# Performance work log

Measured on AMD Instinct MI355X. Metric: run time of the kernel, lower is better.

The kernel has to match this reference:

```python
import jax, jax.numpy as jnp
import numpy as np

B, N, E = 8, 20000, 320000
T, A, P = 4000, 8000, 8000
F_IN, C = 128, 128
N1 = N + 1  # row 0 is a reserved zero/eps node


def setup_inputs() -> dict:
    key = jax.random.key(0)
    ks = jax.random.split(key, 20)
    xn = lambda k, s: jax.random.normal(k, s, dtype=jnp.float32)

    def lin(k, i, o):
        k1, k2 = jax.random.split(k)
        s = (2.0 / (i + o)) ** 0.5  # xavier_normal as in the torch init
        return xn(k1, (i, o)) * s, xn(k2, (o,)) * 0.01

    inp = {}
    inp["topic_emb"] = xn(ks[0], (B, T, 130))
    inp["au_emb"] = xn(ks[1], (B, A, 37))
    inp["paper_emb"] = xn(ks[2], (B, P, 289))
    # disjoint node-id sets covering rows 1..N of feat
    inp["topic_set"] = jnp.broadcast_to(jnp.arange(1, T + 1), (B, T))
    inp["author_set"] = jnp.broadcast_to(jnp.arange(T + 1, T + A + 1), (B, A))
    inp["paper_set"] = jnp.broadcast_to(jnp.arange(T + A + 1, N + 1), (B, P))
    inp["edge_index"] = jax.random.randint(ks[3], (B, 2, E), 1, N + 1)
    inp["topic_id"] = jax.random.randint(ks[4], (B, 50), 1, T + 1)
    inp["author_id"] = jax.random.randint(ks[5], (B, 20), T + 1, T + A + 1)
    inp["topic_cnt"] = jnp.full((B,), 50.0, dtype=jnp.float32)
    inp["auth_cnt"] = jnp.full((B,), 20.0, dtype=jnp.float32)
    # learned params (stored as [in, out], i.e. torch W transposed)
    inp["W_topic"], inp["b_topic"] = lin(ks[6], 130, F_IN)
    inp["W_au"], inp["b_au"] = lin(ks[7], 37, F_IN)
    inp["W_paper"], inp["b_paper"] = lin(ks[8], 289, F_IN)
    inp["gat_W"] = xn(ks[9], (F_IN, C)) * (2.0 / (F_IN + C)) ** 0.5
    inp["att_src"] = xn(ks[10], (C,)) * 0.1
    inp["att_dst"] = xn(ks[11], (C,)) * 0.1
    inp["gat_b"] = jnp.zeros((C,), dtype=jnp.float32)
    inp["W1"], inp["b1"] = lin(ks[12], 3 * C, 2 * C)
    inp["W2"], inp["b2"] = lin(ks[13], 2 * C, C)
    inp["W3"], inp["b3"] = lin(ks[14], C, 1)
    return inp


def reference(topic_emb, au_emb, paper_emb, topic_cnt, auth_cnt,
              W_topic, b_topic, W_au, b_au, W_paper, b_paper,
              gat_W, att_src, att_dst, gat_b,
              W1, b1, W2, b2, W3, b3,
              topic_set, author_set, paper_set, edge_index, topic_id, author_id):
    # eval mode: all dropouts are identity
    t_f = topic_emb @ W_topic + b_topic    # [B,T,F]
    a_f = au_emb @ W_au + b_au             # [B,A,F]
    p_f = paper_emb @ W_paper + b_paper    # [B,P,F]
    loop_idx = jnp.arange(N1)

    def per_graph(tf, af, pf, tset, aset, pset, ei, tid, aid, tcnt, acnt):
        feat = jnp.zeros((N1, F_IN), dtype=tf.dtype)
        feat = feat.at[tset].set(tf).at[aset].set(af).at[pset].set(pf)
        # --- GATConv (heads=1, PyG semantics, self-loops added) ---
        x = feat @ gat_W  # [N1, C]
        src = jnp.concatenate([ei[0], loop_idx])
        dst = jnp.concatenate([ei[1], loop_idx])
        e = jax.nn.leaky_relu((x @ att_src)[src] + (x @ att_dst)[dst], 0.2)
        emax = jax.ops.segment_max(e, dst, num_segments=N1)  # softmax over dst neighborhoods
        ee = jnp.exp(e - emax[dst])
        denom = jax.ops.segment_sum(ee, dst, num_segments=N1) + 1e-16
        out = jax.ops.segment_sum(ee[:, None] * x[src], dst, num_segments=N1) / denom[:, None] + gat_b
        h = jax.nn.relu(out)
        h = h.at[0].set(1e-5)
        # --- gather-sum pooling ---
        t_pool = h[tid].sum(0) / (1e-5 + tcnt)               # [C]
        af2 = h[aid]                                          # [n_auth, C]
        a_pool = jnp.concatenate([af2[0], af2[1:].sum(0) / (-1.00001 + acnt)])  # [2C]
        return jnp.concatenate([a_pool, t_pool])              # [3C]

    cat = jax.vmap(per_graph)(t_f, a_f, p_f, topic_set, author_set, paper_set,
                              edge_index, topic_id, author_id, topic_cnt, auth_cnt)
    h = jnp.tanh(cat @ W1 + b1)
    h = jnp.tanh(h @ W2 + b2)
    return (h @ W3 + b3).reshape(-1)
```

## Files before the change

### kernel.cpp

```cpp
#include <hip/hip_runtime.h>
#include <math.h>

#define BB 8
#define N1 20001
#define TT 4000
#define AAU 8000
#define PP 8000
#define EE 320000
#define CC 128
#define KT 130
#define KA 37
#define KP 289
#define ROWS (KT + KA + KP)
#define CAP 96
#define NS 70
#define EB 128

__device__ __forceinline__ void node_ref(int node, int& t, int& K, int& base, int& row) {
    if (node <= TT)            { t = 0; K = KT; base = 0;        row = node - 1; }
    else if (node <= TT + AAU) { t = 1; K = KA; base = KT;       row = node - TT - 1; }
    else                       { t = 2; K = KP; base = KT + KA;  row = node - TT - AAU - 1; }
}

__device__ __forceinline__ int typ3(int id) { return id <= TT ? 0 : (id <= TT + AAU ? 1 : 2); }
__device__ __forceinline__ float lrelu02(float v) { return v >= 0.f ? v : 0.2f * v; }
__device__ __forceinline__ unsigned hashid(int id) { return (((unsigned)id * 2654435761u) >> 22) & 511u; }

template <int K>
__device__ __forceinline__ float dotK(const float* __restrict__ er,
                                      const float* __restrict__ u, int l) {
    float p = 0.f;
#pragma unroll
    for (int j = 0; j < (K + 63) / 64; ++j) {
        int k = l + 64 * j;
        if (k < K) p += er[k] * u[k];
    }
    return p;
}

template <int K>
__device__ __forceinline__ void dot2K(const float* __restrict__ er,
                                      const float* __restrict__ ul,
                                      const float* __restrict__ udg, int l,
                                      float& ps, float& pd) {
#pragma unroll
    for (int j = 0; j < (K + 63) / 64; ++j) {
        int k = l + 64 * j;
        if (k < K) { float v = er[k]; ps += v * ul[k]; pd += v * udg[k]; }
    }
}

template <int K>
__device__ __forceinline__ void accK(const float* __restrict__ er,
                                     float* __restrict__ z, float w, int l) {
#pragma unroll
    for (int j = 0; j < (K + 63) / 64; ++j) {
        int k = l + 64 * j;
        if (k < K) atomicAdd(&z[k], w * er[k]);
    }
}

__global__ void __launch_bounds__(512)
kPrep(const float* __restrict__ Wt, const float* __restrict__ Wa, const float* __restrict__ Wpp,
      const float* __restrict__ bt, const float* __restrict__ ba, const float* __restrict__ bpw,
      const float* __restrict__ gatW, const float* __restrict__ attS, const float* __restrict__ attD,
      const int* __restrict__ topic_id, const int* __restrict__ author_id,
      float* __restrict__ Wp, float* __restrict__ bp,
      float* __restrict__ u_src, float* __restrict__ u_dst, float* __restrict__ c_sd,
      int* __restrict__ slot_node, int* __restrict__ tid_slot, int* __restrict__ aid_slot,
      int* __restrict__ cnt2) {
    __shared__ int hkey[512], hval[512];
    __shared__ float redS[8], redD[8];
    int bid = blockIdx.x, tid = threadIdx.x;
    if (bid < 115) {
        int c = tid & 127;
        int r = bid * 4 + (tid >> 7);
        float acc = 0.f;
        const float* wrow = nullptr;
        if (r < KT)            wrow = Wt  + (size_t)r * CC;
        else if (r < KT + KA)  wrow = Wa  + (size_t)(r - KT) * CC;
        else if (r < ROWS)     wrow = Wpp + (size_t)(r - KT - KA) * CC;
        else if (r == ROWS)     wrow = bt;
        else if (r == ROWS + 1) wrow = ba;
        else if (r == ROWS + 2) wrow = bpw;
        if (wrow) {
#pragma unroll 16
            for (int j = 0; j < CC; ++j) acc += wrow[j] * gatW[j * CC + c];
            if (r < ROWS) Wp[r * CC + c] = acc;
            else          bp[(r - ROWS) * CC + c] = acc;
        }
        float ps = acc * attS[c], pd = acc * attD[c];
        for (int o = 32; o; o >>= 1) { ps += __shfl_down(ps, o); pd += __shfl_down(pd, o); }
        int w = tid >> 6;
        if ((tid & 63) == 0) { redS[w] = ps; redD[w] = pd; }
        __syncthreads();
        if (tid < 4) {
            int r2 = bid * 4 + tid;
            float us = redS[2 * tid] + redS[2 * tid + 1];
            float ud = redD[2 * tid] + redD[2 * tid + 1];
            if (r2 < ROWS)          { u_src[r2] = us; u_dst[r2] = ud; }
            else if (r2 < ROWS + 3) { c_sd[r2 - ROWS] = us; c_sd[3 + r2 - ROWS] = ud; }
        }
    } else {
        int b = bid - 115;
        for (int i = tid; i < 512; i += 512) { hkey[i] = -1; hval[i] = 0x7fffffff; }
        if (tid < NS) cnt2[b * NS + tid] = 0;
        __syncthreads();
        int id = -1, cell = -1;
        if (tid < NS) {
            id = (tid < 50) ? topic_id[b * 50 + tid] : author_id[b * 20 + tid - 50];
            unsigned h = hashid(id);
            while (true) {
                int old = atomicCAS(&hkey[h], -1, id);
                if (old == -1 || old == id) { cell = (int)h; break; }
                h = (h + 1) & 511u;
            }
            atomicMin(&hval[cell], tid);
        }
        __syncthreads();
        if (tid < NS) {
            int winner = hval[cell];
            if (tid < 50) tid_slot[b * 50 + tid] = winner;
            else          aid_slot[b * 20 + tid - 50] = winner;
            slot_node[b * NS + tid] = (winner == tid) ? id : -1;
        }
    }
}

__global__ void __launch_bounds__(256)
kEdges(const int* __restrict__ edge_index, const int* __restrict__ slot_node,
       int* __restrict__ cnt2, int* __restrict__ entry_src) {
    __shared__ int htab[512];
    int bid = blockIdx.x, b = bid >> 7, chunk = bid & 127, tid = threadIdx.x;
    for (int i = tid; i < 512; i += 256) htab[i] = -1;
    __syncthreads();
    if (tid < NS) {
        int id = slot_node[b * NS + tid];
        if (id >= 0) {
            unsigned h = hashid(id);
            while (atomicCAS(&htab[h], -1, (id << 7) | tid) != -1) h = (h + 1) & 511u;
        }
    }
    __syncthreads();
    const int* dsts  = edge_index + (size_t)b * 2 * EE + EE;
    const int* srcsg = edge_index + (size_t)b * 2 * EE;
    const int per = EE / EB;
    int e0 = chunk * per;
    for (int e = e0 + tid; e < e0 + per; e += 256) {
        int dst = dsts[e];
        unsigned h = hashid(dst);
        int slot = -1;
        while (true) {
            int v = htab[h];
            if (v == -1) break;
            if ((v >> 7) == dst) { slot = v & 127; break; }
            h = (h + 1) & 511u;
        }
        if (slot >= 0) {
            int pos = atomicAdd(&cnt2[b * NS + slot], 1);
            if (pos < CAP) entry_src[(size_t)(b * NS + slot) * CAP + pos] = srcsg[e];
        }
    }
}

__global__ void __launch_bounds__(512)
kAgg(const float* __restrict__ temb, const float* __restrict__ aemb,
     const float* __restrict__ pemb,
     const int* __restrict__ slot_node, const int* __restrict__ cnt2,
     const int* __restrict__ entry_src,
     const float* __restrict__ u_src, const float* __restrict__ u_dst,
     const float* __restrict__ c_sd,
     const float* __restrict__ Wp, const float* __restrict__ bp,
     const float* __restrict__ gatB, float* __restrict__ h_slot) {
    __shared__ float u_l[ROWS], e_l[CAP], w_l[CAP], z_l[ROWS], red_l[4 * CC];
    __shared__ float sw_l[3], s_denom, s_wself, s_asrc, s_adraw;
    int bid = blockIdx.x, b = bid / NS;
    int node = slot_node[bid];
    if (node < 0) return;
    int tid = threadIdx.x, wv = tid >> 6, l = tid & 63;
    int deg = cnt2[bid]; if (deg > CAP) deg = CAP;
    const int* srcs = entry_src + (size_t)bid * CAP;
    const float* tb = temb + (size_t)b * TT * KT;
    const float* ab = aemb + (size_t)b * AAU * KA;
    const float* pb = pemb + (size_t)b * PP * KP;

    for (int i = tid; i < ROWS; i += 512) { u_l[i] = u_src[i]; z_l[i] = 0.f; }
    __syncthreads();

    for (int i = wv; i <= deg; i += 8) {
        int src = (i < deg) ? srcs[i] : node;
        int t, K, base, row; node_ref(src, t, K, base, row);
        const float* er = (t == 0) ? tb + (size_t)row * KT
                        : (t == 1) ? ab + (size_t)row * KA
                                   : pb + (size_t)row * KP;
        if (i < deg) {
            float p;
            if (t == 0)      p = dotK<KT>(er, u_l, l);
            else if (t == 1) p = dotK<KA>(er, u_l + KT, l);
            else             p = dotK<KP>(er, u_l + KT + KA, l);
            for (int o = 32; o; o >>= 1) p += __shfl_down(p, o);
            if (l == 0) e_l[i] = p + c_sd[t];
        } else {
            float ps = 0.f, pd = 0.f;
            if (t == 0)      dot2K<KT>(er, u_l, u_dst, l, ps, pd);
            else if (t == 1) dot2K<KA>(er, u_l + KT, u_dst + KT, l, ps, pd);
            else             dot2K<KP>(er, u_l + KT + KA, u_dst + KT + KA, l, ps, pd);
            for (int o = 32; o; o >>= 1) { ps += __shfl_down(ps, o); pd += __shfl_down(pd, o); }
            if (l == 0) { s_asrc = ps + c_sd[t]; s_adraw = pd + c_sd[3 + t]; }
        }
    }
    __syncthreads();

    if (wv == 0) {
        float adst = s_adraw;
        float es = lrelu02(s_asrc + adst);
        float v0 = (l < deg) ? lrelu02(e_l[l] + adst) : -1e30f;
        float v1 = (l + 64 < deg) ? lrelu02(e_l[l + 64] + adst) : -1e30f;
        float m = fmaxf(v0, v1);
        for (int o = 32; o; o >>= 1) m = fmaxf(m, __shfl_down(m, o));
        m = fmaxf(__shfl(m, 0), es);
        float w0 = 0.f, w1 = 0.f;
        int t0 = 0, t1 = 0;
        if (l < deg)      { w0 = expf(v0 - m); w_l[l] = w0;      t0 = typ3(srcs[l]); }
        if (l + 64 < deg) { w1 = expf(v1 - m); w_l[l + 64] = w1; t1 = typ3(srcs[l + 64]); }
        float s0 = 0.f, s1 = 0.f, s2 = 0.f, d = w0 + w1;
        if (t0 == 0) s0 += w0; else if (t0 == 1) s1 += w0; else s2 += w0;
        if (t1 == 0) s0 += w1; else if (t1 == 1) s1 += w1; else s2 += w1;
        for (int o = 32; o; o >>= 1) {
            d  += __shfl_down(d, o);
            s0 += __shfl_down(s0, o);
            s1 += __shfl_down(s1, o);
            s2 += __shfl_down(s2, o);
        }
        if (l == 0) {
            float ws = expf(es - m);
            d += ws;
            int tn = typ3(node);
            if (tn == 0) s0 += ws; else if (tn == 1) s1 += ws; else s2 += ws;
            sw_l[0] = s0; sw_l[1] = s1; sw_l[2] = s2;
            s_denom = d + 1e-16f;
            s_wself = ws;
        }
    }
    __syncthreads();

    for (int i = wv; i <= deg; i += 8) {
        int src; float w;
        if (i < deg) { src = srcs[i]; w = w_l[i]; }
        else         { src = node;    w = s_wself; }
        int t, K, base, row; node_ref(src, t, K, base, row);
        if (t == 0)      accK<KT>(tb + (size_t)row * KT, z_l, w, l);
        else if (t == 1) accK<KA>(ab + (size_t)row * KA, z_l + KT, w, l);
        else             accK<KP>(pb + (size_t)row * KP, z_l + KT + KA, w, l);
    }
    __syncthreads();

    {
        int kc = tid >> 7, c = tid & 127;
        const int kb = kc * 114, ke = kb + 114;
        float p = 0.f;
#pragma unroll 8
        for (int k = kb; k < ke; ++k) p += z_l[k] * Wp[k * CC + c];
        red_l[kc * CC + c] = p;
    }
    __syncthreads();
    if (tid < CC) {
        float num = red_l[tid] + red_l[CC + tid] + red_l[2 * CC + tid] + red_l[3 * CC + tid];
        num += sw_l[0] * bp[tid] + sw_l[1] * bp[CC + tid] + sw_l[2] * bp[2 * CC + tid];
        float h = num / s_denom + gatB[tid];
        h_slot[(size_t)bid * CC + tid] = h > 0.f ? h : 0.f;
    }
}

__global__ void __launch_bounds__(512)
kPool(const float* __restrict__ h_slot, const int* __restrict__ tid_slot,
      const int* __restrict__ aid_slot,
      const float* __restrict__ tcnt, const float* __restrict__ acnt,
      const float* __restrict__ W1, const float* __restrict__ b1,
      const float* __restrict__ W2, const float* __restrict__ b2,
      const float* __restrict__ W3, const float* __restrict__ b3,
      float* __restrict__ out) {
    __shared__ float cat_l[384], h1_l[256], h2_l[128], redA[2 * 256], redB[4 * 128];
    int b = blockIdx.x, tid = threadIdx.x;
    if (tid < 128) {
        cat_l[tid] = h_slot[(size_t)(b * NS + aid_slot[b * 20]) * CC + tid];
    } else if (tid < 256) {
        int t = tid - 128;
        float ap = 0.f;
        for (int j = 1; j < 20; ++j) ap += h_slot[(size_t)(b * NS + aid_slot[b * 20 + j]) * CC + t];
        cat_l[128 + t] = ap / (acnt[b] - 1.00001f);
    } else if (tid < 384) {
        int t = tid - 256;
        float tp = 0.f;
        for (int j = 0; j < 50; ++j) tp += h_slot[(size_t)(b * NS + tid_slot[b * 50 + j]) * CC + t];
        cat_l[256 + t] = tp / (1e-5f + tcnt[b]);
    }
    __syncthreads();
    {
        int c = tid & 255, half = tid >> 8;
        const int kb = half * 192, ke = kb + 192;
        float acc = 0.f;
#pragma unroll 8
        for (int k = kb; k < ke; ++k) acc += cat_l[k] * W1[k * 256 + c];
        redA[half * 256 + c] = acc;
    }
    __syncthreads();
    if (tid < 256) h1_l[tid] = tanhf(b1[tid] + redA[tid] + redA[256 + tid]);
    __syncthreads();
    {
        int c = tid & 127, q = tid >> 7;
        const int kb = q * 64, ke = kb + 64;
        float acc = 0.f;
#pragma unroll 8
        for (int k = kb; k < ke; ++k) acc += h1_l[k] * W2[k * CC + c];
        redB[q * CC + c] = acc;
    }
    __syncthreads();
    if (tid < 128) {
        float v = tanhf(b2[tid] + redB[tid] + redB[CC + tid] + redB[2 * CC + tid] + redB[3 * CC + tid]);
        h2_l[tid] = v * W3[tid];
    }
    __syncthreads();
    if (tid < 64) {
        float s = h2_l[tid] + h2_l[tid + 64];
        for (int o = 32; o; o >>= 1) s += __shfl_down(s, o);
        if (tid == 0) out[b] = s + b3[0];
    }
}

extern "C" void kernel_launch(void* const* d_in, const int* in_sizes, int n_in,
                              void* d_out, int out_size, void* d_ws, size_t ws_size,
                              hipStream_t stream) {
    const float* temb = (const float*)d_in[0];
    const float* aemb = (const float*)d_in[1];
    const float* pemb = (const float*)d_in[2];
    const int* edge_index = (const int*)d_in[6];
    const int* topic_id   = (const int*)d_in[7];
    const int* author_id  = (const int*)d_in[8];
    const float* tcnt = (const float*)d_in[9];
    const float* acnt = (const float*)d_in[10];
    const float* Wt  = (const float*)d_in[11];
    const float* bt  = (const float*)d_in[12];
    const float* Wa  = (const float*)d_in[13];
    const float* ba  = (const float*)d_in[14];
    const float* Wpw = (const float*)d_in[15];
    const float* bpw = (const float*)d_in[16];
    const float* gatW = (const float*)d_in[17];
    const float* attS = (const float*)d_in[18];
    const float* attD = (const float*)d_in[19];
    const float* gatB = (const float*)d_in[20];
    const float* W1 = (const float*)d_in[21];
    const float* b1 = (const float*)d_in[22];
    const float* W2 = (const float*)d_in[23];
    const float* b2 = (const float*)d_in[24];
    const float* W3 = (const float*)d_in[25];
    const float* b3 = (const float*)d_in[26];

    char* ws = (char*)d_ws;
    size_t off = 0;
    auto alloc = [&](size_t bytes) -> void* {
        void* p = ws + off;
        off = (off + bytes + 255) & ~(size_t)255;
        return p;
    };
    float* Wp      = (float*)alloc((size_t)ROWS * CC * 4);
    float* bp      = (float*)alloc(3 * CC * 4);
    float* u_src   = (float*)alloc(ROWS * 4);
    float* u_dst   = (float*)alloc(ROWS * 4);
    float* c_sd    = (float*)alloc(6 * 4);
    int* slot_node = (int*)alloc(BB * NS * 4);
    int* tid_slot  = (int*)alloc(BB * 50 * 4);
    int* aid_slot  = (int*)alloc(BB * 20 * 4);
    int* cnt2      = (int*)alloc(BB * NS * 4);
    int* entry_src = (int*)alloc((size_t)BB * NS * CAP * 4);
    float* h_slot  = (float*)alloc((size_t)BB * NS * CC * 4);
    (void)ws_size; (void)in_sizes; (void)n_in; (void)out_size;

    kPrep<<<dim3(115 + BB), dim3(512), 0, stream>>>(Wt, Wa, Wpw, bt, ba, bpw, gatW, attS, attD,
                                                    topic_id, author_id,
                                                    Wp, bp, u_src, u_dst, c_sd,
                                                    slot_node, tid_slot, aid_slot, cnt2);
    kEdges<<<dim3(BB * EB), dim3(256), 0, stream>>>(edge_index, slot_node, cnt2, entry_src);
    kAgg<<<dim3(BB * NS), dim3(512), 0, stream>>>(temb, aemb, pemb, slot_node, cnt2, entry_src,
                                                  u_src, u_dst, c_sd, Wp, bp, gatB, h_slot);
    kPool<<<dim3(BB), dim3(512), 0, stream>>>(h_slot, tid_slot, aid_slot, tcnt, acnt,
                                              W1, b1, W2, b2, W3, b3, (float*)d_out);
}
```

Measured before the change: 65.29 us.

## Fuse GAT pipeline into two kernels with per-chunk edge bins and single-pass softmax

Four launches become two. Edge binning moves into the prep kernel: each edge block rebuilds the slot hash table locally and counts into shared-memory bins per chunk, which removes the global atomics on cnt2. Aggregation computes exp weights in a single pass without subtracting the segment max, keeps each row in registers for both the dot product and the weighted accumulation, and fuses the pooling MLP through a last-block-done counter. This cuts launch gaps and extra passes over rows, at the risk of exp overflow for large attention logits and of dropping edges if a chunk bin exceeds 12 entries.

```diff
diff --git a/kernel.cpp b/kernel.cpp
--- a/kernel.cpp
+++ b/kernel.cpp
@@ -2,7 +2,6 @@
 #include <math.h>
 
 #define BB 8
-#define N1 20001
 #define TT 4000
 #define AAU 8000
 #define PP 8000
@@ -11,10 +10,12 @@
 #define KT 130
 #define KA 37
 #define KP 289
-#define ROWS (KT + KA + KP)
-#define CAP 96
+#define ROWS 456
 #define NS 70
-#define EB 128
+#define EBK 64
+#define EPC (EE/EBK)
+#define CAPC 12
+#define NWB 115
 
 __device__ __forceinline__ void node_ref(int node, int& t, int& K, int& base, int& row) {
     if (node <= TT)            { t = 0; K = KT; base = 0;        row = node - 1; }
@@ -22,64 +23,60 @@
     else                       { t = 2; K = KP; base = KT + KA;  row = node - TT - AAU - 1; }
 }
 
-__device__ __forceinline__ int typ3(int id) { return id <= TT ? 0 : (id <= TT + AAU ? 1 : 2); }
 __device__ __forceinline__ float lrelu02(float v) { return v >= 0.f ? v : 0.2f * v; }
 __device__ __forceinline__ unsigned hashid(int id) { return (((unsigned)id * 2654435761u) >> 22) & 511u; }
 
 template <int K>
-__device__ __forceinline__ float dotK(const float* __restrict__ er,
-                                      const float* __restrict__ u, int l) {
+__device__ __forceinline__ void loadRow(const float* __restrict__ er, int l, float* v) {
+#pragma unroll
+    for (int j = 0; j < (K + 63) / 64; ++j) {
+        int k = l + 64 * j;
+        v[j] = (k < K) ? er[k] : 0.f;
+    }
+}
+
+template <int K>
+__device__ __forceinline__ float dotRegs(const float* v, const float* __restrict__ u, int l) {
     float p = 0.f;
 #pragma unroll
     for (int j = 0; j < (K + 63) / 64; ++j) {
         int k = l + 64 * j;
-        if (k < K) p += er[k] * u[k];
+        if (k < K) p += v[j] * u[k];
     }
     return p;
 }
 
 template <int K>
-__device__ __forceinline__ void dot2K(const float* __restrict__ er,
-                                      const float* __restrict__ ul,
-                                      const float* __restrict__ udg, int l,
-                                      float& ps, float& pd) {
+__device__ __forceinline__ void accRegs(const float* v, float* __restrict__ z, float w, int l) {
 #pragma unroll
     for (int j = 0; j < (K + 63) / 64; ++j) {
         int k = l + 64 * j;
-        if (k < K) { float v = er[k]; ps += v * ul[k]; pd += v * udg[k]; }
-    }
-}
-
-template <int K>
-__device__ __forceinline__ void accK(const float* __restrict__ er,
-                                     float* __restrict__ z, float w, int l) {
-#pragma unroll
-    for (int j = 0; j < (K + 63) / 64; ++j) {
-        int k = l + 64 * j;
-        if (k < K) atomicAdd(&z[k], w * er[k]);
+        if (k < K) atomicAdd(&z[k], w * v[j]);
     }
 }
 
 __global__ void __launch_bounds__(512)
-kPrep(const float* __restrict__ Wt, const float* __restrict__ Wa, const float* __restrict__ Wpp,
-      const float* __restrict__ bt, const float* __restrict__ ba, const float* __restrict__ bpw,
-      const float* __restrict__ gatW, const float* __restrict__ attS, const float* __restrict__ attD,
-      const int* __restrict__ topic_id, const int* __restrict__ author_id,
-      float* __restrict__ Wp, float* __restrict__ bp,
-      float* __restrict__ u_src, float* __restrict__ u_dst, float* __restrict__ c_sd,
-      int* __restrict__ slot_node, int* __restrict__ tid_slot, int* __restrict__ aid_slot,
-      int* __restrict__ cnt2) {
-    __shared__ int hkey[512], hval[512];
+k1(const float* __restrict__ Wt, const float* __restrict__ Wa, const float* __restrict__ Wpp,
+   const float* __restrict__ bt, const float* __restrict__ ba, const float* __restrict__ bpw,
+   const float* __restrict__ gatW, const float* __restrict__ attS, const float* __restrict__ attD,
+   const int* __restrict__ topic_id, const int* __restrict__ author_id,
+   const int* __restrict__ edge_index,
+   float* __restrict__ Wp, float* __restrict__ bp,
+   float* __restrict__ u_src, float* __restrict__ u_dst, float* __restrict__ c_sd,
+   int* __restrict__ slot_node, int* __restrict__ tid_slot, int* __restrict__ aid_slot,
+   int* __restrict__ cnt2, int* __restrict__ entry_src, int* __restrict__ done) {
+    __shared__ int hkey[512], hval[512], lcnt[NS];
     __shared__ float redS[8], redD[8];
     int bid = blockIdx.x, tid = threadIdx.x;
-    if (bid < 115) {
+
+    if (bid < NWB) {
         int c = tid & 127;
         int r = bid * 4 + (tid >> 7);
         float acc = 0.f;
         const float* wrow = nullptr;
-        if (r < KT)            wrow = Wt  + (size_t)r * CC;
-        else if (r < KT + KA)  wrow = Wa  + (size_t)(r - KT) * CC;
-        else if (r < ROWS)     wrow = Wpp + (size_t)(r - KT - KA) * CC;
+        if (r < KT)             wrow = Wt  + (size_t)r * CC;
+        else if (r < KT + KA)   wrow = Wa  + (size_t)(r - KT) * CC;
+        else if (r < ROWS)      wrow = Wpp + (size_t)(r - KT - KA) * CC;
         else if (r == ROWS)     wrow = bt;
         else if (r == ROWS + 1) wrow = ba;
         else if (r == ROWS + 2) wrow = bpw;
@@ -101,10 +98,10 @@
             if (r2 < ROWS)          { u_src[r2] = us; u_dst[r2] = ud; }
             else if (r2 < ROWS + 3) { c_sd[r2 - ROWS] = us; c_sd[3 + r2 - ROWS] = ud; }
         }
-    } else {
-        int b = bid - 115;
+    } else if (bid < NWB + BB) {
+        int b = bid - NWB;
         for (int i = tid; i < 512; i += 512) { hkey[i] = -1; hval[i] = 0x7fffffff; }
-        if (tid < NS) cnt2[b * NS + tid] = 0;
+        if (tid == 0) done[b] = 0;
         __syncthreads();
         int id = -1, cell = -1;
         if (tid < NS) {
@@ -124,207 +121,194 @@
             else          aid_slot[b * 20 + tid - 50] = winner;
             slot_node[b * NS + tid] = (winner == tid) ? id : -1;
         }
-    }
-}
-
-__global__ void __launch_bounds__(256)
-kEdges(const int* __restrict__ edge_index, const int* __restrict__ slot_node,
-       int* __restrict__ cnt2, int* __restrict__ entry_src) {
-    __shared__ int htab[512];
-    int bid = blockIdx.x, b = bid >> 7, chunk = bid & 127, tid = threadIdx.x;
-    for (int i = tid; i < 512; i += 256) htab[i] = -1;
-    __syncthreads();
-    if (tid < NS) {
-        int id = slot_node[b * NS + tid];
-        if (id >= 0) {
+    } else {
+        int eb = bid - NWB - BB;
+        int b = eb / EBK, chunk = eb % EBK;
+        for (int i = tid; i < 512; i += 512) { hkey[i] = -1; hval[i] = 0x7fffffff; }
+        if (tid < NS) lcnt[tid] = 0;
+        __syncthreads();
+        if (tid < NS) {
+            int id = (tid < 50) ? topic_id[b * 50 + tid] : author_id[b * 20 + tid - 50];
             unsigned h = hashid(id);
-            while (atomicCAS(&htab[h], -1, (id << 7) | tid) != -1) h = (h + 1) & 511u;
-        }
-    }
-    __syncthreads();
-    const int* dsts  = edge_index + (size_t)b * 2 * EE + EE;
-    const int* srcsg = edge_index + (size_t)b * 2 * EE;
-    const int per = EE / EB;
-    int e0 = chunk * per;
-    for (int e = e0 + tid; e < e0 + per; e += 256) {
-        int dst = dsts[e];
-        unsigned h = hashid(dst);
-        int slot = -1;
-        while (true) {
-            int v = htab[h];
-            if (v == -1) break;
-            if ((v >> 7) == dst) { slot = v & 127; break; }
-            h = (h + 1) & 511u;
-        }
-        if (slot >= 0) {
-            int pos = atomicAdd(&cnt2[b * NS + slot], 1);
-            if (pos < CAP) entry_src[(size_t)(b * NS + slot) * CAP + pos] = srcsg[e];
+            int cell;
+            while (true) {
+                int old = atomicCAS(&hkey[h], -1, id);
+                if (old == -1 || old == id) { cell = (int)h; break; }
+                h = (h + 1) & 511u;
+            }
+            atomicMin(&hval[cell], tid);
+        }
+        __syncthreads();
+        const int* dsts = edge_index + (size_t)b * 2 * EE + EE + (size_t)chunk * EPC;
+        const int* srcs = edge_index + (size_t)b * 2 * EE + (size_t)chunk * EPC;
+        for (int e = tid; e < EPC; e += 512) {
+            int dst = dsts[e];
+            unsigned h = hashid(dst);
+            int slot = -1;
+            while (true) {
+                int k = hkey[h];
+                if (k == -1) break;
+                if (k == dst) { slot = hval[h]; break; }
+                h = (h + 1) & 511u;
+            }
+            if (slot >= 0) {
+                int pos = atomicAdd(&lcnt[slot], 1);
+                if (pos < CAPC) entry_src[((size_t)(b * NS + slot) * EBK + chunk) * CAPC + pos] = srcs[e];
+            }
+        }
+        __syncthreads();
+        if (tid < NS) {
+            int cn = lcnt[tid]; if (cn > CAPC) cn = CAPC;
+            cnt2[(size_t)(b * NS + tid) * EBK + chunk] = cn;
         }
     }
 }
 
 __global__ void __launch_bounds__(512)
-kAgg(const float* __restrict__ temb, const float* __restrict__ aemb,
-     const float* __restrict__ pemb,
-     const int* __restrict__ slot_node, const int* __restrict__ cnt2,
-     const int* __restrict__ entry_src,
-     const float* __restrict__ u_src, const float* __restrict__ u_dst,
-     const float* __restrict__ c_sd,
-     const float* __restrict__ Wp, const float* __restrict__ bp,
-     const float* __restrict__ gatB, float* __restrict__ h_slot) {
-    __shared__ float u_l[ROWS], e_l[CAP], w_l[CAP], z_l[ROWS], red_l[4 * CC];
-    __shared__ float sw_l[3], s_denom, s_wself, s_asrc, s_adraw;
+k2(const float* __restrict__ temb, const float* __restrict__ aemb, const float* __restrict__ pemb,
+   const int* __restrict__ slot_node, const int* __restrict__ cnt2, const int* __restrict__ entry_src,
+   const float* __restrict__ u_src, const float* __restrict__ u_dst, const float* __restrict__ c_sd,
+   const float* __restrict__ Wp, const float* __restrict__ bp, const float* __restrict__ gatB,
+   const int* __restrict__ tid_slot, const int* __restrict__ aid_slot,
+   const float* __restrict__ tcnt, const float* __restrict__ acnt,
+   const float* __restrict__ W1, const float* __restrict__ b1,
+   const float* __restrict__ W2, const float* __restrict__ b2,
+   const float* __restrict__ W3, const float* __restrict__ b3,
+   float* __restrict__ h_slot, int* __restrict__ done, float* __restrict__ out) {
+    __shared__ float S[1920];
+    __shared__ int counts_l[EBK];
+    __shared__ float csd_l[6], misc[4];
+    __shared__ int s_ret;
+    float* u_l  = S;
+    float* ud_l = S + 456;
+    float* z_l  = S + 912;
+    float* red  = S + 1368;
+
     int bid = blockIdx.x, b = bid / NS;
+    int tid = threadIdx.x, wv = tid >> 6, l = tid & 63;
     int node = slot_node[bid];
-    if (node < 0) return;
-    int tid = threadIdx.x, wv = tid >> 6, l = tid & 63;
-    int deg = cnt2[bid]; if (deg > CAP) deg = CAP;
-    const int* srcs = entry_src + (size_t)bid * CAP;
-    const float* tb = temb + (size_t)b * TT * KT;
-    const float* ab = aemb + (size_t)b * AAU * KA;
-    const float* pb = pemb + (size_t)b * PP * KP;
-
-    for (int i = tid; i < ROWS; i += 512) { u_l[i] = u_src[i]; z_l[i] = 0.f; }
-    __syncthreads();
-
-    for (int i = wv; i <= deg; i += 8) {
-        int src = (i < deg) ? srcs[i] : node;
-        int t, K, base, row; node_ref(src, t, K, base, row);
-        const float* er = (t == 0) ? tb + (size_t)row * KT
-                        : (t == 1) ? ab + (size_t)row * KA
-                                   : pb + (size_t)row * KP;
-        if (i < deg) {
-            float p;
-            if (t == 0)      p = dotK<KT>(er, u_l, l);
-            else if (t == 1) p = dotK<KA>(er, u_l + KT, l);
-            else             p = dotK<KP>(er, u_l + KT + KA, l);
-            for (int o = 32; o; o >>= 1) p += __shfl_down(p, o);
-            if (l == 0) e_l[i] = p + c_sd[t];
-        } else {
+
+    for (int i = tid; i < ROWS; i += 512) { u_l[i] = u_src[i]; ud_l[i] = u_dst[i]; z_l[i] = 0.f; }
+    if (tid < EBK) counts_l[tid] = cnt2[(size_t)bid * EBK + tid];
+    if (tid < 6) csd_l[tid] = c_sd[tid];
+    if (tid < 4) misc[tid] = 0.f;
+    __syncthreads();
+
+    if (node >= 0) {
+        const float* tb = temb + (size_t)b * TT * KT;
+        const float* ab = aemb + (size_t)b * AAU * KA;
+        const float* pb = pemb + (size_t)b * PP * KP;
+        float v[5];
+        float adraw;
+        {
+            int t, K, base, row; node_ref(node, t, K, base, row);
             float ps = 0.f, pd = 0.f;
-            if (t == 0)      dot2K<KT>(er, u_l, u_dst, l, ps, pd);
-            else if (t == 1) dot2K<KA>(er, u_l + KT, u_dst + KT, l, ps, pd);
-            else             dot2K<KP>(er, u_l + KT + KA, u_dst + KT + KA, l, ps, pd);
-            for (int o = 32; o; o >>= 1) { ps += __shfl_down(ps, o); pd += __shfl_down(pd, o); }
-            if (l == 0) { s_asrc = ps + c_sd[t]; s_adraw = pd + c_sd[3 + t]; }
-        }
-    }
-    __syncthreads();
-
-    if (wv == 0) {
-        float adst = s_adraw;
-        float es = lrelu02(s_asrc + adst);
-        float v0 = (l < deg) ? lrelu02(e_l[l] + adst) : -1e30f;
-        float v1 = (l + 64 < deg) ? lrelu02(e_l[l + 64] + adst) : -1e30f;
-        float m = fmaxf(v0, v1);
-        for (int o = 32; o; o >>= 1) m = fmaxf(m, __shfl_down(m, o));
-        m = fmaxf(__shfl(m, 0), es);
-        float w0 = 0.f, w1 = 0.f;
-        int t0 = 0, t1 = 0;
-        if (l < deg)      { w0 = expf(v0 - m); w_l[l] = w0;      t0 = typ3(srcs[l]); }
-        if (l + 64 < deg) { w1 = expf(v1 - m); w_l[l + 64] = w1; t1 = typ3(srcs[l + 64]); }
-        float s0 = 0.f, s1 = 0.f, s2 = 0.f, d = w0 + w1;
-        if (t0 == 0) s0 += w0; else if (t0 == 1) s1 += w0; else s2 += w0;
-        if (t1 == 0) s0 += w1; else if (t1 == 1) s1 += w1; else s2 += w1;
-        for (int o = 32; o; o >>= 1) {
-            d  += __shfl_down(d, o);
-            s0 += __shfl_down(s0, o);
-            s1 += __shfl_down(s1, o);
-            s2 += __shfl_down(s2, o);
-        }
-        if (l == 0) {
-            float ws = expf(es - m);
-            d += ws;
-            int tn = typ3(node);
-            if (tn == 0) s0 += ws; else if (tn == 1) s1 += ws; else s2 += ws;
-            sw_l[0] = s0; sw_l[1] = s1; sw_l[2] = s2;
-            s_denom = d + 1e-16f;
-            s_wself = ws;
-        }
-    }
-    __syncthreads();
-
-    for (int i = wv; i <= deg; i += 8) {
-        int src; float w;
-        if (i < deg) { src = srcs[i]; w = w_l[i]; }
-        else         { src = node;    w = s_wself; }
-        int t, K, base, row; node_ref(src, t, K, base, row);
-        if (t == 0)      accK<KT>(tb + (size_t)row * KT, z_l, w, l);
-        else if (t == 1) accK<KA>(ab + (size_t)row * KA, z_l + KT, w, l);
-        else             accK<KP>(pb + (size_t)row * KP, z_l + KT + KA, w, l);
-    }
-    __syncthreads();
-
-    {
+            if (t == 0)      { const float* er = tb + (size_t)row * KT; loadRow<KT>(er, l, v); ps = dotRegs<KT>(v, u_l, l);          pd = dotRegs<KT>(v, ud_l, l); }
+            else if (t == 1) { const float* er = ab + (size_t)row * KA; loadRow<KA>(er, l, v); ps = dotRegs<KA>(v, u_l + KT, l);     pd = dotRegs<KA>(v, ud_l + KT, l); }
+            else             { const float* er = pb + (size_t)row * KP; loadRow<KP>(er, l, v); ps = dotRegs<KP>(v, u_l + KT + KA, l); pd = dotRegs<KP>(v, ud_l + KT + KA, l); }
+            for (int o = 32; o; o >>= 1) { ps += __shfl_xor(ps, o); pd += __shfl_xor(pd, o); }
+            float asrc = ps + csd_l[t];
+            adraw = pd + csd_l[3 + t];
+            float wself = expf(lrelu02(asrc + adraw));
+            if (wv == 0) {
+                if (t == 0)      accRegs<KT>(v, z_l, wself, l);
+                else if (t == 1) accRegs<KA>(v, z_l + KT, wself, l);
+                else             accRegs<KP>(v, z_l + KT + KA, wself, l);
+                if (l == 0) { atomicAdd(&misc[0], wself); atomicAdd(&misc[1 + t], wself); }
+            }
+        }
+        for (int chunk = wv; chunk < EBK; chunk += 8) {
+            int cn = counts_l[chunk];
+            const int* ep = entry_src + ((size_t)bid * EBK + chunk) * CAPC;
+            for (int j = 0; j < cn; ++j) {
+                int src = ep[j];
+                int t, K, base, row; node_ref(src, t, K, base, row);
+                float p = 0.f;
+                if (t == 0)      { const float* er = tb + (size_t)row * KT; loadRow<KT>(er, l, v); p = dotRegs<KT>(v, u_l, l); }
+                else if (t == 1) { const float* er = ab + (size_t)row * KA; loadRow<KA>(er, l, v); p = dotRegs<KA>(v, u_l + KT, l); }
+                else             { const float* er = pb + (size_t)row * KP; loadRow<KP>(er, l, v); p = dotRegs<KP>(v, u_l + KT + KA, l); }
+                for (int o = 32; o; o >>= 1) p += __shfl_xor(p, o);
+                float w = expf(lrelu02(p + csd_l[t] + adraw));
+                if (t == 0)      accRegs<KT>(v, z_l, w, l);
+                else if (t == 1) accRegs<KA>(v, z_l + KT, w, l);
+                else             accRegs<KP>(v, z_l + KT + KA, w, l);
+                if (l == 0) { atomicAdd(&misc[0], w); atomicAdd(&misc[1 + t], w); }
+            }
+        }
+    }
+    __syncthreads();
+
+    if (node >= 0) {
         int kc = tid >> 7, c = tid & 127;
         const int kb = kc * 114, ke = kb + 114;
         float p = 0.f;
 #pragma unroll 8
         for (int k = kb; k < ke; ++k) p += z_l[k] * Wp[k * CC + c];
-        red_l[kc * CC + c] = p;
-    }
-    __syncthreads();
-    if (tid < CC) {
-        float num = red_l[tid] + red_l[CC + tid] + red_l[2 * CC + tid] + red_l[3 * CC + tid];
-        num += sw_l[0] * bp[tid] + sw_l[1] * bp[CC + tid] + sw_l[2] * bp[2 * CC + tid];
-        float h = num / s_denom + gatB[tid];
+        red[kc * CC + c] = p;
+    }
+    __syncthreads();
+    if (node >= 0 && tid < CC) {
+        float num = red[tid] + red[CC + tid] + red[2 * CC + tid] + red[3 * CC + tid];
+        num += misc[1] * bp[tid] + misc[2] * bp[CC + tid] + misc[3] * bp[2 * CC + tid];
+        float h = num / misc[0] + gatB[tid];
         h_slot[(size_t)bid * CC + tid] = h > 0.f ? h : 0.f;
     }
-}
-
-__global__ void __launch_bounds__(512)
-kPool(const float* __restrict__ h_slot, const int* __restrict__ tid_slot,
-      const int* __restrict__ aid_slot,
-      const float* __restrict__ tcnt, const float* __restrict__ acnt,
-      const float* __restrict__ W1, const float* __restrict__ b1,
-      const float* __restrict__ W2, const float* __restrict__ b2,
-      const float* __restrict__ W3, const float* __restrict__ b3,
-      float* __restrict__ out) {
-    __shared__ float cat_l[384], h1_l[256], h2_l[128], redA[2 * 256], redB[4 * 128];
-    int b = blockIdx.x, tid = threadIdx.x;
-    if (tid < 128) {
-        cat_l[tid] = h_slot[(size_t)(b * NS + aid_slot[b * 20]) * CC + tid];
-    } else if (tid < 256) {
-        int t = tid - 128;
-        float ap = 0.f;
-        for (int j = 1; j < 20; ++j) ap += h_slot[(size_t)(b * NS + aid_slot[b * 20 + j]) * CC + t];
-        cat_l[128 + t] = ap / (acnt[b] - 1.00001f);
-    } else if (tid < 384) {
-        int t = tid - 256;
-        float tp = 0.f;
-        for (int j = 0; j < 50; ++j) tp += h_slot[(size_t)(b * NS + tid_slot[b * 50 + j]) * CC + t];
-        cat_l[256 + t] = tp / (1e-5f + tcnt[b]);
-    }
-    __syncthreads();
-    {
-        int c = tid & 255, half = tid >> 8;
-        const int kb = half * 192, ke = kb + 192;
-        float acc = 0.f;
+    __threadfence();
+    __syncthreads();
+    if (tid == 0) s_ret = atomicAdd(&done[b], 1);
+    __syncthreads();
+
+    if (s_ret == NS - 1) {
+        __threadfence();
+        float* cat = S;
+        float* h1  = S + 384;
+        float* h2  = S + 640;
+        float* rA  = S + 768;
+        float* rB  = S + 1280;
+        if (tid < 128) {
+            cat[tid] = h_slot[(size_t)(b * NS + aid_slot[b * 20]) * CC + tid];
+        } else if (tid < 256) {
+            int t = tid - 128;
+            float ap = 0.f;
+            for (int j = 1; j < 20; ++j) ap += h_slot[(size_t)(b * NS + aid_slot[b * 20 + j]) * CC + t];
+            cat[128 + t] = ap / (acnt[b] - 1.00001f);
+        } else if (tid < 384) {
+            int t = tid - 256;
+            float tp = 0.f;
+            for (int j = 0; j < 50; ++j) tp += h_slot[(size_t)(b * NS + tid_slot[b * 50 + j]) * CC + t];
+            cat[256 + t] = tp / (1e-5f + tcnt[b]);
+        }
+        __syncthreads();
+        {
+            int c = tid & 255, half = tid >> 8;
+            const int kb = half * 192, ke = kb + 192;
+            float acc = 0.f;
 #pragma unroll 8
-        for (int k = kb; k < ke; ++k) acc += cat_l[k] * W1[k * 256 + c];
-        redA[half * 256 + c] = acc;
-    }
-    __syncthreads();
-    if (tid < 256) h1_l[tid] = tanhf(b1[tid] + redA[tid] + redA[256 + tid]);
-    __syncthreads();
-    {
-        int c = tid & 127, q = tid >> 7;
-        const int kb = q * 64, ke = kb + 64;
-        float acc = 0.f;
+            for (int k = kb; k < ke; ++k) acc += cat[k] * W1[k * 256 + c];
+            rA[half * 256 + c] = acc;
+        }
+        __syncthreads();
+        if (tid < 256) h1[tid] = tanhf(b1[tid] + rA[tid] + rA[256 + tid]);
+        __syncthreads();
+        {
+            int c = tid & 127, q = tid >> 7;
+            const int kb = q * 64, ke = kb + 64;
+            float acc = 0.f;
 #pragma unroll 8
-        for (int k = kb; k < ke; ++k) acc += h1_l[k] * W2[k * CC + c];
-        redB[q * CC + c] = acc;
-    }
-    __syncthreads();
-    if (tid < 128) {
-        float v = tanhf(b2[tid] + redB[tid] + redB[CC + tid] + redB[2 * CC + tid] + redB[3 * CC + tid]);
-        h2_l[tid] = v * W3[tid];
-    }
-    __syncthreads();
-    if (tid < 64) {
-        float s = h2_l[tid] + h2_l[tid + 64];
-        for (int o = 32; o; o >>= 1) s += __shfl_down(s, o);
-        if (tid == 0) out[b] = s + b3[0];
+            for (int k = kb; k < ke; ++k) acc += h1[k] * W2[k * CC + c];
+            rB[q * CC + c] = acc;
+        }
+        __syncthreads();
+        if (tid < 128) {
+            float vv = tanhf(b2[tid] + rB[tid] + rB[CC + tid] + rB[2 * CC + tid] + rB[3 * CC + tid]);
+            h2[tid] = vv * W3[tid];
+        }
+        __syncthreads();
+        if (tid < 64) {
+            float s = h2[tid] + h2[tid + 64];
+            for (int o = 32; o; o >>= 1) s += __shfl_down(s, o);
+            if (tid == 0) out[b] = s + b3[0];
+        }
     }
 }
 
@@ -371,18 +355,21 @@
     int* slot_node = (int*)alloc(BB * NS * 4);
     int* tid_slot  = (int*)alloc(BB * 50 * 4);
     int* aid_slot  = (int*)alloc(BB * 20 * 4);
-    int* cnt2      = (int*)alloc(BB * NS * 4);
-    int* entry_src = (int*)alloc((size_t)BB * NS * CAP * 4);
+    int* cnt2      = (int*)alloc((size_t)BB * NS * EBK * 4);
+    int* entry_src = (int*)alloc((size_t)BB * NS * EBK * CAPC * 4);
+    int* done      = (int*)alloc(BB * 4);
     float* h_slot  = (float*)alloc((size_t)BB * NS * CC * 4);
     (void)ws_size; (void)in_sizes; (void)n_in; (void)out_size;
 
-    kPrep<<<dim3(115 + BB), dim3(512), 0, stream>>>(Wt, Wa, Wpw, bt, ba, bpw, gatW, attS, attD,
-                                                    topic_id, author_id,
-                                                    Wp, bp, u_src, u_dst, c_sd,
-                                                    slot_node, tid_slot, aid_slot, cnt2);
-    kEdges<<<dim3(BB * EB), dim3(256), 0, stream>>>(edge_index, slot_node, cnt2, entry_src);
-    kAgg<<<dim3(BB * NS), dim3(512), 0, stream>>>(temb, aemb, pemb, slot_node, cnt2, entry_src,
-                                                  u_src, u_dst, c_sd, Wp, bp, gatB, h_slot);
-    kPool<<<dim3(BB), dim3(512), 0, stream>>>(h_slot, tid_slot, aid_slot, tcnt, acnt,
-                                              W1, b1, W2, b2, W3, b3, (float*)d_out);
-}
+    k1<<<dim3(NWB + BB + BB * EBK), dim3(512), 0, stream>>>(
+        Wt, Wa, Wpw, bt, ba, bpw, gatW, attS, attD,
+        topic_id, author_id, edge_index,
+        Wp, bp, u_src, u_dst, c_sd,
+        slot_node, tid_slot, aid_slot, cnt2, entry_src, done);
+    k2<<<dim3(BB * NS), dim3(512), 0, stream>>>(
+        temb, aemb, pemb, slot_node, cnt2, entry_src,
+        u_src, u_dst, c_sd, Wp, bp, gatB,
+        tid_slot, aid_slot, tcnt, acnt,
+        W1, b1, W2, b2, W3, b3,
+        h_slot, done, (float*)d_out);
+}
```

After: 121.1 us. +85.4%, slower.
